# Kernel tuning notes

Hardware: AMD Instinct MI355X
Metric: run time of the kernel (lower is better)

Reference implementation:

```python
import jax, jax.numpy as jnp
import numpy as np

N = 50000          # nodes
E = 1600000        # edges (avg degree 32)
B = 64             # graphs in batch
IN_CH = 128
HEADS = 8
HD = 8             # head_dim = ceil(64/8)
GH = HEADS * HD    # 64 = gat_hidden_dim
HIDDEN = 64
NC = 10
NEG_SLOPE = 0.2
BN_EPS = 1e-5
SIGMA = 0.5


def setup_inputs() -> dict:
    key = jax.random.key(0)
    ks = jax.random.split(key, 24)
    s = 0.1
    inp = {
        "x": jax.random.normal(ks[0], (N, IN_CH), jnp.float32),
        "raw_x": jax.random.uniform(ks[1], (N, 3), jnp.float32),
        "edge_index": jax.random.randint(ks[2], (2, E), 0, N, jnp.int32),
        "batch": jnp.sort(jax.random.randint(ks[3], (N,), 0, B, jnp.int32)),
        # conv1 (heads=8, out=8, edge_dim=1)
        "W1": jax.random.normal(ks[4], (IN_CH, GH), jnp.float32) * s,
        "att_src1": jax.random.normal(ks[5], (HEADS, HD), jnp.float32) * s,
        "att_dst1": jax.random.normal(ks[6], (HEADS, HD), jnp.float32) * s,
        "We1": jax.random.normal(ks[7], (1, GH), jnp.float32) * s,
        "att_e1": jax.random.normal(ks[8], (HEADS, HD), jnp.float32) * s,
        "b1": jax.random.normal(ks[9], (GH,), jnp.float32) * s,
        "gamma1": jnp.ones((GH,), jnp.float32),
        "beta1": jnp.zeros((GH,), jnp.float32),
        "rm1": jax.random.normal(ks[10], (GH,), jnp.float32) * s,
        "rv1": jax.random.uniform(ks[11], (GH,), jnp.float32) + 0.5,
        # conv2 (heads=1, out=64, edge_dim=1)
        "W2": jax.random.normal(ks[12], (GH, HIDDEN), jnp.float32) * s,
        "att_src2": jax.random.normal(ks[13], (1, HIDDEN), jnp.float32) * s,
        "att_dst2": jax.random.normal(ks[14], (1, HIDDEN), jnp.float32) * s,
        "We2": jax.random.normal(ks[15], (1, HIDDEN), jnp.float32) * s,
        "att_e2": jax.random.normal(ks[16], (1, HIDDEN), jnp.float32) * s,
        "b2": jax.random.normal(ks[17], (HIDDEN,), jnp.float32) * s,
        "gamma2": jnp.ones((HIDDEN,), jnp.float32),
        "beta2": jnp.zeros((HIDDEN,), jnp.float32),
        "rm2": jax.random.normal(ks[18], (HIDDEN,), jnp.float32) * s,
        "rv2": jax.random.uniform(ks[19], (HIDDEN,), jnp.float32) + 0.5,
        # classifier
        "Wc": jax.random.normal(ks[20], (HIDDEN, NC), jnp.float32) * s,
        "bc": jax.random.normal(ks[21], (NC,), jnp.float32) * s,
    }
    return inp


def _gat_conv(x, src, dst, edge_attr, W, a_src, a_dst, W_e, a_e, bias, heads, out_ch, n):
    """PyG GATConv (concat=True, add_self_loops=True, fill_value='mean', eval mode)."""
    e0 = edge_attr.shape[0]
    # self-loop edge_attr = mean of incoming edge_attr per node (0 if isolated)
    cnt = jax.ops.segment_sum(jnp.ones((e0,), x.dtype), dst, num_segments=n)
    loop_attr = jax.ops.segment_sum(edge_attr, dst, num_segments=n) / jnp.maximum(cnt, 1.0)[:, None]
    loops = jnp.arange(n, dtype=src.dtype)
    src2 = jnp.concatenate([src, loops])
    dst2 = jnp.concatenate([dst, loops])
    ea = jnp.concatenate([edge_attr, loop_attr], axis=0)          # [E2, 1]
    h = (x @ W).reshape(n, heads, out_ch)                          # [N, H, D]
    al_s = (h * a_src).sum(-1)                                     # [N, H]
    al_d = (h * a_dst).sum(-1)                                     # [N, H]
    al_e = ((ea @ W_e).reshape(-1, heads, out_ch) * a_e).sum(-1)   # [E2, H]
    logits = al_s[src2] + al_d[dst2] + al_e                        # [E2, H]
    logits = jnp.where(logits >= 0, logits, NEG_SLOPE * logits)    # leaky_relu
    # segment softmax over destination nodes (every node has a self loop)
    m = jax.ops.segment_max(logits, dst2, num_segments=n)
    ex = jnp.exp(logits - m[dst2])
    alpha = ex / jax.ops.segment_sum(ex, dst2, num_segments=n)[dst2]
    out = jax.ops.segment_sum(h[src2] * alpha[:, :, None], dst2, num_segments=n)
    return out.reshape(n, heads * out_ch) + bias


def _bn_eval(x, gamma, beta, rm, rv):
    return (x - rm) * (gamma / jnp.sqrt(rv + BN_EPS)) + beta


def reference(x, raw_x, edge_index, batch,
              W1, att_src1, att_dst1, We1, att_e1, b1, gamma1, beta1, rm1, rv1,
              W2, att_src2, att_dst2, We2, att_e2, b2, gamma2, beta2, rm2, rv2,
              Wc, bc):
    src, dst = edge_index[0], edge_index[1]
    # gaussian edge weights from raw features
    diff = raw_x[src] - raw_x[dst]
    dist2 = (diff * diff).sum(axis=1)
    edge_w = jnp.exp(-dist2 / (2.0 * SIGMA * SIGMA))[:, None]      # [E, 1]
    # eval mode: dropout is identity
    h = _gat_conv(x, src, dst, edge_w, W1, att_src1, att_dst1, We1, att_e1, b1, HEADS, HD, N)
    h = jax.nn.elu(_bn_eval(h, gamma1, beta1, rm1, rv1))
    h = _gat_conv(h, src, dst, edge_w, W2, att_src2, att_dst2, We2, att_e2, b2, 1, HIDDEN, N)
    h = jax.nn.elu(_bn_eval(h, gamma2, beta2, rm2, rv2))
    # global mean pool over graphs
    cnt = jax.ops.segment_sum(jnp.ones((N,), h.dtype), batch, num_segments=B)
    g = jax.ops.segment_sum(h, batch, num_segments=B) / jnp.maximum(cnt, 1.0)[:, None]
    return g @ Wc + bc
```

## Files before the change

kernel.cpp:

```cpp
#include <hip/hip_runtime.h>
#include <math.h>

#define N_NODES 50000
#define N_EDGES 1600000
#define NBATCH  64
#define INCH    128
#define HEADS   8
#define HD      8
#define GH      64
#define HIDDEN  64
#define NC      10
#define NEG_SLOPE 0.2f
#define BN_EPS  1e-5f

#define SCAN_TPB 1024
#define NTILES   ((N_NODES + SCAN_TPB - 1) / SCAN_TPB)

typedef unsigned short ushort_t;
typedef unsigned int uint_t;

__device__ __forceinline__ ushort_t f2bf(float f) {
  uint_t u = __float_as_uint(f);
  uint_t r = (u + 0x7fffu + ((u >> 16) & 1u)) >> 16;
  return (ushort_t)r;
}
__device__ __forceinline__ float2 upk(uint_t u) {
  return make_float2(__uint_as_float(u << 16), __uint_as_float(u & 0xffff0000u));
}

__global__ __launch_bounds__(256) void edge_kernel(
    const int* __restrict__ ei, const float* __restrict__ raw,
    float* __restrict__ ea, float* __restrict__ easum, int* __restrict__ cnt) {
  int e = blockIdx.x * blockDim.x + threadIdx.x;
  if (e >= N_EDGES) return;
  int s = ei[e], d = ei[N_EDGES + e];
  float dx = raw[s*3+0] - raw[d*3+0];
  float dy = raw[s*3+1] - raw[d*3+1];
  float dz = raw[s*3+2] - raw[d*3+2];
  float w = __expf(-2.0f * (dx*dx + dy*dy + dz*dz));
  ea[e] = w;
  atomicAdd(&easum[d], w);
  atomicAdd(&cnt[d], 1);
}

__global__ __launch_bounds__(SCAN_TPB) void scan_part(
    const int* __restrict__ cnt, const float* __restrict__ easum,
    int* __restrict__ rowptr, float* __restrict__ loopat, int* __restrict__ bsum) {
  __shared__ int s[SCAN_TPB];
  int t = threadIdx.x;
  int i = blockIdx.x * SCAN_TPB + t;
  int v = (i < N_NODES) ? cnt[i] : 0;
  s[t] = v; __syncthreads();
  for (int off = 1; off < SCAN_TPB; off <<= 1) {
    int u = (t >= off) ? s[t - off] : 0;
    __syncthreads();
    s[t] += u;
    __syncthreads();
  }
  if (i < N_NODES) {
    rowptr[i] = s[t] - v;
    loopat[i] = easum[i] / fmaxf((float)v, 1.0f);
  }
  if (t == SCAN_TPB - 1) bsum[blockIdx.x] = s[t];
}

__global__ __launch_bounds__(64) void scan_top(int* __restrict__ bsum, int* __restrict__ rowptr) {
  int t = threadIdx.x;
  int v = (t < NTILES) ? bsum[t] : 0;
  int orig = v;
  for (int off = 1; off < 64; off <<= 1) {
    int u = __shfl_up(v, off);
    if (t >= off) v += u;
  }
  if (t < NTILES) bsum[t] = v - orig;
  if (t == 0) rowptr[N_NODES] = N_EDGES;
}

__global__ __launch_bounds__(SCAN_TPB) void scan_add(int* __restrict__ rowptr, const int* __restrict__ bsum) {
  int i = blockIdx.x * SCAN_TPB + threadIdx.x;
  if (i < N_NODES) rowptr[i] += bsum[blockIdx.x];
}

__global__ __launch_bounds__(256) void scatter_kernel(
    const int* __restrict__ ei, const float* __restrict__ ea,
    const int* __restrict__ rowptr, int* __restrict__ cnt2,
    int* __restrict__ csr_src, float* __restrict__ csr_ea) {
  int e = blockIdx.x * blockDim.x + threadIdx.x;
  if (e >= N_EDGES) return;
  int s = ei[e], d = ei[N_EDGES + e];
  int pos = rowptr[d] + atomicAdd(&cnt2[d], 1);
  csr_src[pos] = s;
  csr_ea[pos] = ea[e];
}

__global__ __launch_bounds__(256) void gemm1_kernel(
    const float* __restrict__ x, const float* __restrict__ W1,
    const float* __restrict__ asrc, const float* __restrict__ adst,
    ushort_t* __restrict__ h1b, float* __restrict__ als, float* __restrict__ ald) {
  __shared__ float w[INCH * GH];
  for (int i = threadIdx.x; i < INCH * GH / 4; i += blockDim.x)
    ((float4*)w)[i] = ((const float4*)W1)[i];
  __syncthreads();
  int lane = threadIdx.x & 63;
  int waveG = __builtin_amdgcn_readfirstlane((blockIdx.x * blockDim.x + threadIdx.x) >> 6);
  int nWaves = (gridDim.x * blockDim.x) >> 6;
  float a_s = asrc[lane];
  float a_d = adst[lane];
  for (int base = waveG * 4; base < N_NODES; base += nWaves * 4) {
    float acc[4] = {0.f, 0.f, 0.f, 0.f};
    #pragma unroll 8
    for (int k = 0; k < INCH; ++k) {
      float wv = w[k * GH + lane];
      #pragma unroll
      for (int j = 0; j < 4; ++j)
        acc[j] = fmaf(x[(size_t)(base + j) * INCH + k], wv, acc[j]);
    }
    #pragma unroll
    for (int j = 0; j < 4; ++j) {
      int n = base + j;
      float hv = acc[j];
      h1b[(size_t)n * GH + lane] = f2bf(hv);
      float ps = hv * a_s, pd = hv * a_d;
      ps += __shfl_xor(ps, 1); ps += __shfl_xor(ps, 2); ps += __shfl_xor(ps, 4);
      pd += __shfl_xor(pd, 1); pd += __shfl_xor(pd, 2); pd += __shfl_xor(pd, 4);
      if ((lane & 7) == 0) {
        als[n * HEADS + (lane >> 3)] = ps;
        ald[n * HEADS + (lane >> 3)] = pd;
      }
    }
  }
}

__global__ __launch_bounds__(256) void conv1_kernel(
    const ushort_t* __restrict__ h1b, const float* __restrict__ als,
    const float* __restrict__ ald,
    const float* __restrict__ We, const float* __restrict__ ae,
    const int* __restrict__ rowptr,
    const int* __restrict__ csr_src, const float* __restrict__ csr_ea,
    const float* __restrict__ loopat, const float* __restrict__ bias,
    const float* __restrict__ gamma, const float* __restrict__ beta,
    const float* __restrict__ rm, const float* __restrict__ rv,
    float* __restrict__ h2) {
  __shared__ int   src_lds[4][64];
  __shared__ float ea_lds[4][64];
  int l = threadIdx.x & 63;
  int w = threadIdx.x >> 6;
  int n = blockIdx.x * 4 + w;
  if (n >= N_NODES) return;
  int i = l & 15;
  int q = l >> 4;
  int head = i >> 1;
  float4 we4 = ((const float4*)We)[i];
  float4 ae4 = ((const float4*)ae)[i];
  float ce = we4.x*ae4.x + we4.y*ae4.y + we4.z*ae4.z + we4.w*ae4.w;
  ce += __shfl_xor(ce, 1);
  float aldn = ald[(size_t)n * HEADS + head];
  float als_self = als[(size_t)n * HEADS + head];
  const uint2* tab = (const uint2*)h1b;
  uint2 uself = tab[(size_t)n * 16 + i];
  float2 s01 = upk(uself.x), s23 = upk(uself.y);
  int jb = rowptr[n], je = rowptr[n + 1];
  float ssum = 0.f;
  float a0 = 0.f, a1 = 0.f, a2 = 0.f, a3 = 0.f;

#define C1_LOADS(J, R, A, E)                                           \
  {                                                                    \
    int jj = (J);                                                      \
    bool vv = jj < cnt;                                                \
    int ss = vv ? src_lds[w][jj] : 0;                                  \
    R = tab[(size_t)ss * 16 + i];                                      \
    A = vv ? als[(size_t)ss * HEADS + head] : -1e30f;                  \
    E = vv ? ea_lds[w][jj] : 0.f;                                      \
  }
#define C1_LOADG(GI, R0,R1,R2,R3, A0,A1,A2,A3, E0,E1,E2,E3)            \
  {                                                                    \
    int jbase = (GI) * 16 + q;                                         \
    C1_LOADS(jbase,      R0, A0, E0)                                   \
    C1_LOADS(jbase + 4,  R1, A1, E1)                                   \
    C1_LOADS(jbase + 8,  R2, A2, E2)                                   \
    C1_LOADS(jbase + 12, R3, A3, E3)                                   \
  }
#define C1_PROC(R, A, E)                                               \
  {                                                                    \
    float2 t01 = upk(R.x), t23 = upk(R.y);                             \
    float lg = A + aldn + E * ce;                                      \
    lg = (lg >= 0.f) ? lg : NEG_SLOPE * lg;                            \
    float p = __expf(fminf(lg, 60.f));                                 \
    ssum += p;                                                         \
    a0 = fmaf(p, t01.x, a0); a1 = fmaf(p, t01.y, a1);                  \
    a2 = fmaf(p, t23.x, a2); a3 = fmaf(p, t23.y, a3);                  \
  }

  for (int cb = jb; cb < je; cb += 64) {
    int cnt = je - cb; if (cnt > 64) cnt = 64;
    src_lds[w][l] = (l < cnt) ? csr_src[cb + l] : 0;
    ea_lds[w][l]  = (l < cnt) ? csr_ea[cb + l] : 0.f;
    int ng = (cnt + 15) >> 4;
    uint2 rA0, rA1, rA2, rA3, rB0, rB1, rB2, rB3;
    float aA0, aA1, aA2, aA3, aB0, aB1, aB2, aB3;
    float eA0, eA1, eA2, eA3, eB0, eB1, eB2, eB3;
    C1_LOADG(0, rA0,rA1,rA2,rA3, aA0,aA1,aA2,aA3, eA0,eA1,eA2,eA3)
    for (int gi = 0; gi < ng; gi += 2) {
      bool hasB = (gi + 1) < ng;
      if (hasB) C1_LOADG(gi + 1, rB0,rB1,rB2,rB3, aB0,aB1,aB2,aB3, eB0,eB1,eB2,eB3)
      C1_PROC(rA0, aA0, eA0) C1_PROC(rA1, aA1, eA1)
      C1_PROC(rA2, aA2, eA2) C1_PROC(rA3, aA3, eA3)
      if (hasB) {
        if (gi + 2 < ng) C1_LOADG(gi + 2, rA0,rA1,rA2,rA3, aA0,aA1,aA2,aA3, eA0,eA1,eA2,eA3)
        C1_PROC(rB0, aB0, eB0) C1_PROC(rB1, aB1, eB1)
        C1_PROC(rB2, aB2, eB2) C1_PROC(rB3, aB3, eB3)
      }
    }
  }
#undef C1_LOADS
#undef C1_LOADG
#undef C1_PROC

  ssum += __shfl_xor(ssum, 16); ssum += __shfl_xor(ssum, 32);
  a0 += __shfl_xor(a0, 16); a0 += __shfl_xor(a0, 32);
  a1 += __shfl_xor(a1, 16); a1 += __shfl_xor(a1, 32);
  a2 += __shfl_xor(a2, 16); a2 += __shfl_xor(a2, 32);
  a3 += __shfl_xor(a3, 16); a3 += __shfl_xor(a3, 32);
  {
    float lg = als_self + aldn + loopat[n] * ce;
    lg = (lg >= 0.f) ? lg : NEG_SLOPE * lg;
    float p = __expf(fminf(lg, 60.f));
    ssum += p;
    a0 = fmaf(p, s01.x, a0); a1 = fmaf(p, s01.y, a1);
    a2 = fmaf(p, s23.x, a2); a3 = fmaf(p, s23.y, a3);
  }
  if (q == 0) {
    float inv = 1.0f / ssum;
    float4 b4 = ((const float4*)bias)[i];
    float4 g4 = ((const float4*)gamma)[i];
    float4 be4 = ((const float4*)beta)[i];
    float4 rm4 = ((const float4*)rm)[i];
    float4 rv4 = ((const float4*)rv)[i];
    float o0 = a0 * inv + b4.x, o1 = a1 * inv + b4.y;
    float o2 = a2 * inv + b4.z, o3 = a3 * inv + b4.w;
    o0 = (o0 - rm4.x) * (g4.x * rsqrtf(rv4.x + BN_EPS)) + be4.x;
    o1 = (o1 - rm4.y) * (g4.y * rsqrtf(rv4.y + BN_EPS)) + be4.y;
    o2 = (o2 - rm4.z) * (g4.z * rsqrtf(rv4.z + BN_EPS)) + be4.z;
    o3 = (o3 - rm4.w) * (g4.w * rsqrtf(rv4.w + BN_EPS)) + be4.w;
    o0 = (o0 > 0.f) ? o0 : expm1f(o0);
    o1 = (o1 > 0.f) ? o1 : expm1f(o1);
    o2 = (o2 > 0.f) ? o2 : expm1f(o2);
    o3 = (o3 > 0.f) ? o3 : expm1f(o3);
    ((float4*)(h2 + (size_t)n * GH))[i] = make_float4(o0, o1, o2, o3);
  }
}

__global__ __launch_bounds__(256) void gemm2_kernel(
    const float* __restrict__ x, const float* __restrict__ W2,
    const float* __restrict__ asrc, const float* __restrict__ adst,
    ushort_t* __restrict__ h2mb, float* __restrict__ als, float* __restrict__ ald) {
  __shared__ float w[HIDDEN * HIDDEN];
  for (int i = threadIdx.x; i < HIDDEN * HIDDEN / 4; i += blockDim.x)
    ((float4*)w)[i] = ((const float4*)W2)[i];
  __syncthreads();
  int lane = threadIdx.x & 63;
  int waveG = __builtin_amdgcn_readfirstlane((blockIdx.x * blockDim.x + threadIdx.x) >> 6);
  int nWaves = (gridDim.x * blockDim.x) >> 6;
  float a_s = asrc[lane];
  float a_d = adst[lane];
  for (int base = waveG * 4; base < N_NODES; base += nWaves * 4) {
    float acc[4] = {0.f, 0.f, 0.f, 0.f};
    #pragma unroll 8
    for (int k = 0; k < HIDDEN; ++k) {
      float wv = w[k * HIDDEN + lane];
      #pragma unroll
      for (int j = 0; j < 4; ++j)
        acc[j] = fmaf(x[(size_t)(base + j) * HIDDEN + k], wv, acc[j]);
    }
    #pragma unroll
    for (int j = 0; j < 4; ++j) {
      int n = base + j;
      float hv = acc[j];
      h2mb[(size_t)n * HIDDEN + lane] = f2bf(hv);
      float ps = hv * a_s, pd = hv * a_d;
      #pragma unroll
      for (int off = 1; off < 64; off <<= 1) {
        ps += __shfl_xor(ps, off);
        pd += __shfl_xor(pd, off);
      }
      if (lane == 0) { als[n] = ps; ald[n] = pd; }
    }
  }
}

__global__ __launch_bounds__(256) void conv2_kernel(
    const ushort_t* __restrict__ h2mb, const float* __restrict__ als,
    const float* __restrict__ ald,
    const float* __restrict__ We, const float* __restrict__ ae,
    const int* __restrict__ rowptr,
    const int* __restrict__ csr_src, const float* __restrict__ csr_ea,
    const float* __restrict__ loopat, const float* __restrict__ bias,
    const float* __restrict__ gamma, const float* __restrict__ beta,
    const float* __restrict__ rm, const float* __restrict__ rv,
    const int* __restrict__ batch,
    float* __restrict__ pool, int* __restrict__ cntg) {
  __shared__ int   src_lds[4][64];
  __shared__ float ea_lds[4][64];
  int l = threadIdx.x & 63;
  int w = threadIdx.x >> 6;
  int n = blockIdx.x * 4 + w;
  if (n >= N_NODES) return;
  int i = l & 15;
  int q = l >> 4;
  float4 we4 = ((const float4*)We)[i];
  float4 ae4 = ((const float4*)ae)[i];
  float ce = we4.x*ae4.x + we4.y*ae4.y + we4.z*ae4.z + we4.w*ae4.w;
  ce += __shfl_xor(ce, 1); ce += __shfl_xor(ce, 2);
  ce += __shfl_xor(ce, 4); ce += __shfl_xor(ce, 8);
  float aldn = ald[n];
  float als_self = als[n];
  const uint2* tab = (const uint2*)h2mb;
  uint2 uself = tab[(size_t)n * 16 + i];
  float2 s01 = upk(uself.x), s23 = upk(uself.y);
  int jb = rowptr[n], je = rowptr[n + 1];
  float ssum = 0.f;
  float a0 = 0.f, a1 = 0.f, a2 = 0.f, a3 = 0.f;

#define C2_LOADS(J, R, A, E)                                           \
  {                                                                    \
    int jj = (J);                                                      \
    bool vv = jj < cnt;                                                \
    int ss = vv ? src_lds[w][jj] : 0;                                  \
    R = tab[(size_t)ss * 16 + i];                                      \
    A = vv ? als[ss] : -1e30f;                                         \
    E = vv ? ea_lds[w][jj] : 0.f;                                      \
  }
#define C2_LOADG(GI, R0,R1,R2,R3, A0,A1,A2,A3, E0,E1,E2,E3)            \
  {                                                                    \
    int jbase = (GI) * 16 + q;                                         \
    C2_LOADS(jbase,      R0, A0, E0)                                   \
    C2_LOADS(jbase + 4,  R1, A1, E1)                                   \
    C2_LOADS(jbase + 8,  R2, A2, E2)                                   \
    C2_LOADS(jbase + 12, R3, A3, E3)                                   \
  }
#define C2_PROC(R, A, E)                                               \
  {                                                                    \
    float2 t01 = upk(R.x), t23 = upk(R.y);                             \
    float lg = A + aldn + E * ce;                                      \
    lg = (lg >= 0.f) ? lg : NEG_SLOPE * lg;                            \
    float p = __expf(fminf(lg, 60.f));                                 \
    ssum += p;                                                         \
    a0 = fmaf(p, t01.x, a0); a1 = fmaf(p, t01.y, a1);                  \
    a2 = fmaf(p, t23.x, a2); a3 = fmaf(p, t23.y, a3);                  \
  }

  for (int cb = jb; cb < je; cb += 64) {
    int cnt = je - cb; if (cnt > 64) cnt = 64;
    src_lds[w][l] = (l < cnt) ? csr_src[cb + l] : 0;
    ea_lds[w][l]  = (l < cnt) ? csr_ea[cb + l] : 0.f;
    int ng = (cnt + 15) >> 4;
    uint2 rA0, rA1, rA2, rA3, rB0, rB1, rB2, rB3;
    float aA0, aA1, aA2, aA3, aB0, aB1, aB2, aB3;
    float eA0, eA1, eA2, eA3, eB0, eB1, eB2, eB3;
    C2_LOADG(0, rA0,rA1,rA2,rA3, aA0,aA1,aA2,aA3, eA0,eA1,eA2,eA3)
    for (int gi = 0; gi < ng; gi += 2) {
      bool hasB = (gi + 1) < ng;
      if (hasB) C2_LOADG(gi + 1, rB0,rB1,rB2,rB3, aB0,aB1,aB2,aB3, eB0,eB1,eB2,eB3)
      C2_PROC(rA0, aA0, eA0) C2_PROC(rA1, aA1, eA1)
      C2_PROC(rA2, aA2, eA2) C2_PROC(rA3, aA3, eA3)
      if (hasB) {
        if (gi + 2 < ng) C2_LOADG(gi + 2, rA0,rA1,rA2,rA3, aA0,aA1,aA2,aA3, eA0,eA1,eA2,eA3)
        C2_PROC(rB0, aB0, eB0) C2_PROC(rB1, aB1, eB1)
        C2_PROC(rB2, aB2, eB2) C2_PROC(rB3, aB3, eB3)
      }
    }
  }
#undef C2_LOADS
#undef C2_LOADG
#undef C2_PROC

  ssum += __shfl_xor(ssum, 16); ssum += __shfl_xor(ssum, 32);
  a0 += __shfl_xor(a0, 16); a0 += __shfl_xor(a0, 32);
  a1 += __shfl_xor(a1, 16); a1 += __shfl_xor(a1, 32);
  a2 += __shfl_xor(a2, 16); a2 += __shfl_xor(a2, 32);
  a3 += __shfl_xor(a3, 16); a3 += __shfl_xor(a3, 32);
  {
    float lg = als_self + aldn + loopat[n] * ce;
    lg = (lg >= 0.f) ? lg : NEG_SLOPE * lg;
    float p = __expf(fminf(lg, 60.f));
    ssum += p;
    a0 = fmaf(p, s01.x, a0); a1 = fmaf(p, s01.y, a1);
    a2 = fmaf(p, s23.x, a2); a3 = fmaf(p, s23.y, a3);
  }
  if (q == 0) {
    float inv = 1.0f / ssum;
    float4 b4 = ((const float4*)bias)[i];
    float4 g4 = ((const float4*)gamma)[i];
    float4 be4 = ((const float4*)beta)[i];
    float4 rm4 = ((const float4*)rm)[i];
    float4 rv4 = ((const float4*)rv)[i];
    float o0 = a0 * inv + b4.x, o1 = a1 * inv + b4.y;
    float o2 = a2 * inv + b4.z, o3 = a3 * inv + b4.w;
    o0 = (o0 - rm4.x) * (g4.x * rsqrtf(rv4.x + BN_EPS)) + be4.x;
    o1 = (o1 - rm4.y) * (g4.y * rsqrtf(rv4.y + BN_EPS)) + be4.y;
    o2 = (o2 - rm4.z) * (g4.z * rsqrtf(rv4.z + BN_EPS)) + be4.z;
    o3 = (o3 - rm4.w) * (g4.w * rsqrtf(rv4.w + BN_EPS)) + be4.w;
    o0 = (o0 > 0.f) ? o0 : expm1f(o0);
    o1 = (o1 > 0.f) ? o1 : expm1f(o1);
    o2 = (o2 > 0.f) ? o2 : expm1f(o2);
    o3 = (o3 > 0.f) ? o3 : expm1f(o3);
    int b = batch[n];
    float* pp = pool + (size_t)b * HIDDEN + 4 * i;
    atomicAdd(pp + 0, o0);
    atomicAdd(pp + 1, o1);
    atomicAdd(pp + 2, o2);
    atomicAdd(pp + 3, o3);
    if (l == 0) atomicAdd(&cntg[b], 1);
  }
}

__global__ __launch_bounds__(640) void final_kernel(
    const float* __restrict__ pool, const int* __restrict__ cntg,
    const float* __restrict__ Wc, const float* __restrict__ bc,
    float* __restrict__ out) {
  int t = threadIdx.x;
  if (t >= NBATCH * NC) return;
  int b = t / NC, c = t - b * NC;
  float inv = 1.0f / fmaxf((float)cntg[b], 1.0f);
  float s = bc[c];
  #pragma unroll
  for (int d = 0; d < HIDDEN; ++d)
    s = fmaf(pool[b * HIDDEN + d] * inv, Wc[d * NC + c], s);
  out[t] = s;
}

extern "C" void kernel_launch(void* const* d_in, const int* in_sizes, int n_in,
                              void* d_out, int out_size, void* d_ws, size_t ws_size,
                              hipStream_t stream) {
  const float* x     = (const float*)d_in[0];
  const float* raw   = (const float*)d_in[1];
  const int*   ei    = (const int*)  d_in[2];
  const int*   batch = (const int*)  d_in[3];
  const float* W1    = (const float*)d_in[4];
  const float* asrc1 = (const float*)d_in[5];
  const float* adst1 = (const float*)d_in[6];
  const float* We1   = (const float*)d_in[7];
  const float* ae1   = (const float*)d_in[8];
  const float* b1    = (const float*)d_in[9];
  const float* g1    = (const float*)d_in[10];
  const float* be1   = (const float*)d_in[11];
  const float* rm1   = (const float*)d_in[12];
  const float* rv1   = (const float*)d_in[13];
  const float* W2    = (const float*)d_in[14];
  const float* asrc2 = (const float*)d_in[15];
  const float* adst2 = (const float*)d_in[16];
  const float* We2   = (const float*)d_in[17];
  const float* ae2   = (const float*)d_in[18];
  const float* b2    = (const float*)d_in[19];
  const float* g2    = (const float*)d_in[20];
  const float* be2   = (const float*)d_in[21];
  const float* rm2   = (const float*)d_in[22];
  const float* rv2   = (const float*)d_in[23];
  const float* Wc    = (const float*)d_in[24];
  const float* bc    = (const float*)d_in[25];
  float* out = (float*)d_out;

  char* ws = (char*)d_ws;
  size_t off = 0;
  auto alloc = [&](size_t bytes) -> void* {
    void* p = ws + off;
    off += bytes;
    off = (off + 255) & ~(size_t)255;
    return p;
  };
  float*    ea      = (float*)   alloc((size_t)N_EDGES * 4);
  float*    csr_ea  = (float*)   alloc((size_t)N_EDGES * 4);
  int*      csr_src = (int*)     alloc((size_t)N_EDGES * 4);
  float*    easum   = (float*)   alloc((size_t)N_NODES * 4);
  int*      cnt     = (int*)     alloc((size_t)N_NODES * 4);
  int*      cnt2    = (int*)     alloc((size_t)N_NODES * 4);
  int*      rowptr  = (int*)     alloc((size_t)(N_NODES + 1) * 4);
  float*    loopat  = (float*)   alloc((size_t)N_NODES * 4);
  ushort_t* h1b     = (ushort_t*)alloc((size_t)N_NODES * GH * 2);
  float*    als1    = (float*)   alloc((size_t)N_NODES * HEADS * 4);
  float*    ald1    = (float*)   alloc((size_t)N_NODES * HEADS * 4);
  float*    h2      = (float*)   alloc((size_t)N_NODES * GH * 4);
  ushort_t* h2mb    = (ushort_t*)alloc((size_t)N_NODES * HIDDEN * 2);
  float*    als2    = (float*)   alloc((size_t)N_NODES * 4);
  float*    ald2    = (float*)   alloc((size_t)N_NODES * 4);
  int*      bsum    = (int*)     alloc(64 * 4);
  float*    pool    = (float*)   alloc((size_t)NBATCH * HIDDEN * 4);
  int*      cntg    = (int*)     alloc((size_t)NBATCH * 4);

  hipMemsetAsync(easum, 0, (size_t)N_NODES * 4, stream);
  hipMemsetAsync(cnt,   0, (size_t)N_NODES * 4, stream);
  hipMemsetAsync(cnt2,  0, (size_t)N_NODES * 4, stream);
  hipMemsetAsync(pool,  0, (size_t)NBATCH * HIDDEN * 4, stream);
  hipMemsetAsync(cntg,  0, (size_t)NBATCH * 4, stream);

  int egrid = (N_EDGES + 255) / 256;
  edge_kernel<<<egrid, 256, 0, stream>>>(ei, raw, ea, easum, cnt);
  scan_part<<<NTILES, SCAN_TPB, 0, stream>>>(cnt, easum, rowptr, loopat, bsum);
  scan_top<<<1, 64, 0, stream>>>(bsum, rowptr);
  scan_add<<<NTILES, SCAN_TPB, 0, stream>>>(rowptr, bsum);
  scatter_kernel<<<egrid, 256, 0, stream>>>(ei, ea, rowptr, cnt2, csr_src, csr_ea);

  gemm1_kernel<<<1024, 256, 0, stream>>>(x, W1, asrc1, adst1, h1b, als1, ald1);
  conv1_kernel<<<(N_NODES + 3) / 4, 256, 0, stream>>>(h1b, als1, ald1, We1, ae1,
      rowptr, csr_src, csr_ea, loopat, b1, g1, be1, rm1, rv1, h2);
  gemm2_kernel<<<1024, 256, 0, stream>>>(h2, W2, asrc2, adst2, h2mb, als2, ald2);
  conv2_kernel<<<(N_NODES + 3) / 4, 256, 0, stream>>>(h2mb, als2, ald2, We2, ae2,
      rowptr, csr_src, csr_ea, loopat, b2, g2, be2, rm2, rv2, batch, pool, cntg);
  final_kernel<<<1, 640, 0, stream>>>(pool, cntg, Wc, bc, out);
}
```

Measured before the change: 1.005 ms.

## Split feature gather tables into halves and run conv passes per half

The bf16 node feature tables are split into two 32-column halves, and each GAT aggregation kernel runs twice, once per half. The aim is to shrink the randomly gathered table from 6.4MB to 3.2MB per pass so it fits better in the L2/LLC, cutting miss traffic on neighbor gathers. In exchange, the CSR indices, edge attributes and attention logits are read twice, and each pass recomputes the softmax denominator.

```diff
diff --git a/kernel.cpp b/kernel.cpp
--- a/kernel.cpp
+++ b/kernel.cpp
@@ -96,7 +96,8 @@
 __global__ __launch_bounds__(256) void gemm1_kernel(
     const float* __restrict__ x, const float* __restrict__ W1,
     const float* __restrict__ asrc, const float* __restrict__ adst,
-    ushort_t* __restrict__ h1b, float* __restrict__ als, float* __restrict__ ald) {
+    ushort_t* __restrict__ tabLo, ushort_t* __restrict__ tabHi,
+    float* __restrict__ als, float* __restrict__ ald) {
   __shared__ float w[INCH * GH];
   for (int i = threadIdx.x; i < INCH * GH / 4; i += blockDim.x)
     ((float4*)w)[i] = ((const float4*)W1)[i];
@@ -119,7 +120,9 @@
     for (int j = 0; j < 4; ++j) {
       int n = base + j;
       float hv = acc[j];
-      h1b[(size_t)n * GH + lane] = f2bf(hv);
+      ushort_t hb = f2bf(hv);
+      if (lane < 32) tabLo[(size_t)n * 32 + lane] = hb;
+      else           tabHi[(size_t)n * 32 + (lane - 32)] = hb;
       float ps = hv * a_s, pd = hv * a_d;
       ps += __shfl_xor(ps, 1); ps += __shfl_xor(ps, 2); ps += __shfl_xor(ps, 4);
       pd += __shfl_xor(pd, 1); pd += __shfl_xor(pd, 2); pd += __shfl_xor(pd, 4);
@@ -131,8 +134,8 @@
   }
 }
 
-__global__ __launch_bounds__(256) void conv1_kernel(
-    const ushort_t* __restrict__ h1b, const float* __restrict__ als,
+__global__ __launch_bounds__(256) void conv1_half_kernel(
+    const ushort_t* __restrict__ tab, const float* __restrict__ als,
     const float* __restrict__ ald,
     const float* __restrict__ We, const float* __restrict__ ae,
     const int* __restrict__ rowptr,
@@ -140,47 +143,40 @@
     const float* __restrict__ loopat, const float* __restrict__ bias,
     const float* __restrict__ gamma, const float* __restrict__ beta,
     const float* __restrict__ rm, const float* __restrict__ rv,
-    float* __restrict__ h2) {
+    float* __restrict__ h2, int H) {
   __shared__ int   src_lds[4][64];
   __shared__ float ea_lds[4][64];
   int l = threadIdx.x & 63;
   int w = threadIdx.x >> 6;
   int n = blockIdx.x * 4 + w;
   if (n >= N_NODES) return;
-  int i = l & 15;
-  int q = l >> 4;
-  int head = i >> 1;
-  float4 we4 = ((const float4*)We)[i];
-  float4 ae4 = ((const float4*)ae)[i];
+  int i8 = l & 7;
+  int oct = l >> 3;
+  int fidx = H * 8 + i8;
+  int head = H * 4 + (i8 >> 1);
+  float4 we4 = ((const float4*)We)[fidx];
+  float4 ae4 = ((const float4*)ae)[fidx];
   float ce = we4.x*ae4.x + we4.y*ae4.y + we4.z*ae4.z + we4.w*ae4.w;
   ce += __shfl_xor(ce, 1);
-  float aldn = ald[(size_t)n * HEADS + head];
+  float aldn     = ald[(size_t)n * HEADS + head];
   float als_self = als[(size_t)n * HEADS + head];
-  const uint2* tab = (const uint2*)h1b;
-  uint2 uself = tab[(size_t)n * 16 + i];
+  const uint2* tb = (const uint2*)tab;
+  uint2 uself = tb[(size_t)n * 8 + i8];
   float2 s01 = upk(uself.x), s23 = upk(uself.y);
   int jb = rowptr[n], je = rowptr[n + 1];
   float ssum = 0.f;
   float a0 = 0.f, a1 = 0.f, a2 = 0.f, a3 = 0.f;
 
-#define C1_LOADS(J, R, A, E)                                           \
+#define CH1_LOADG(G, R, A, E)                                          \
   {                                                                    \
-    int jj = (J);                                                      \
+    int jj = (G) * 8 + oct;                                            \
     bool vv = jj < cnt;                                                \
     int ss = vv ? src_lds[w][jj] : 0;                                  \
-    R = tab[(size_t)ss * 16 + i];                                      \
+    R = tb[(size_t)ss * 8 + i8];                                       \
     A = vv ? als[(size_t)ss * HEADS + head] : -1e30f;                  \
     E = vv ? ea_lds[w][jj] : 0.f;                                      \
   }
-#define C1_LOADG(GI, R0,R1,R2,R3, A0,A1,A2,A3, E0,E1,E2,E3)            \
-  {                                                                    \
-    int jbase = (GI) * 16 + q;                                         \
-    C1_LOADS(jbase,      R0, A0, E0)                                   \
-    C1_LOADS(jbase + 4,  R1, A1, E1)                                   \
-    C1_LOADS(jbase + 8,  R2, A2, E2)                                   \
-    C1_LOADS(jbase + 12, R3, A3, E3)                                   \
-  }
-#define C1_PROC(R, A, E)                                               \
+#define CH1_PROC(R, A, E)                                              \
   {                                                                    \
     float2 t01 = upk(R.x), t23 = upk(R.y);                             \
     float lg = A + aldn + E * ce;                                      \
@@ -195,32 +191,27 @@
     int cnt = je - cb; if (cnt > 64) cnt = 64;
     src_lds[w][l] = (l < cnt) ? csr_src[cb + l] : 0;
     ea_lds[w][l]  = (l < cnt) ? csr_ea[cb + l] : 0.f;
-    int ng = (cnt + 15) >> 4;
-    uint2 rA0, rA1, rA2, rA3, rB0, rB1, rB2, rB3;
-    float aA0, aA1, aA2, aA3, aB0, aB1, aB2, aB3;
-    float eA0, eA1, eA2, eA3, eB0, eB1, eB2, eB3;
-    C1_LOADG(0, rA0,rA1,rA2,rA3, aA0,aA1,aA2,aA3, eA0,eA1,eA2,eA3)
-    for (int gi = 0; gi < ng; gi += 2) {
-      bool hasB = (gi + 1) < ng;
-      if (hasB) C1_LOADG(gi + 1, rB0,rB1,rB2,rB3, aB0,aB1,aB2,aB3, eB0,eB1,eB2,eB3)
-      C1_PROC(rA0, aA0, eA0) C1_PROC(rA1, aA1, eA1)
-      C1_PROC(rA2, aA2, eA2) C1_PROC(rA3, aA3, eA3)
+    int ng = (cnt + 7) >> 3;
+    uint2 rA, rB; float aA, aB, eA, eB;
+    CH1_LOADG(0, rA, aA, eA)
+    for (int g = 0; g < ng; g += 2) {
+      bool hasB = (g + 1) < ng;
+      if (hasB) CH1_LOADG(g + 1, rB, aB, eB)
+      CH1_PROC(rA, aA, eA)
       if (hasB) {
-        if (gi + 2 < ng) C1_LOADG(gi + 2, rA0,rA1,rA2,rA3, aA0,aA1,aA2,aA3, eA0,eA1,eA2,eA3)
-        C1_PROC(rB0, aB0, eB0) C1_PROC(rB1, aB1, eB1)
-        C1_PROC(rB2, aB2, eB2) C1_PROC(rB3, aB3, eB3)
+        if (g + 2 < ng) CH1_LOADG(g + 2, rA, aA, eA)
+        CH1_PROC(rB, aB, eB)
       }
     }
   }
-#undef C1_LOADS
-#undef C1_LOADG
-#undef C1_PROC
-
-  ssum += __shfl_xor(ssum, 16); ssum += __shfl_xor(ssum, 32);
-  a0 += __shfl_xor(a0, 16); a0 += __shfl_xor(a0, 32);
-  a1 += __shfl_xor(a1, 16); a1 += __shfl_xor(a1, 32);
-  a2 += __shfl_xor(a2, 16); a2 += __shfl_xor(a2, 32);
-  a3 += __shfl_xor(a3, 16); a3 += __shfl_xor(a3, 32);
+#undef CH1_LOADG
+#undef CH1_PROC
+
+  ssum += __shfl_xor(ssum, 8); ssum += __shfl_xor(ssum, 16); ssum += __shfl_xor(ssum, 32);
+  a0 += __shfl_xor(a0, 8); a0 += __shfl_xor(a0, 16); a0 += __shfl_xor(a0, 32);
+  a1 += __shfl_xor(a1, 8); a1 += __shfl_xor(a1, 16); a1 += __shfl_xor(a1, 32);
+  a2 += __shfl_xor(a2, 8); a2 += __shfl_xor(a2, 16); a2 += __shfl_xor(a2, 32);
+  a3 += __shfl_xor(a3, 8); a3 += __shfl_xor(a3, 16); a3 += __shfl_xor(a3, 32);
   {
     float lg = als_self + aldn + loopat[n] * ce;
     lg = (lg >= 0.f) ? lg : NEG_SLOPE * lg;
@@ -229,13 +220,13 @@
     a0 = fmaf(p, s01.x, a0); a1 = fmaf(p, s01.y, a1);
     a2 = fmaf(p, s23.x, a2); a3 = fmaf(p, s23.y, a3);
   }
-  if (q == 0) {
+  if (oct == 0) {
     float inv = 1.0f / ssum;
-    float4 b4 = ((const float4*)bias)[i];
-    float4 g4 = ((const float4*)gamma)[i];
-    float4 be4 = ((const float4*)beta)[i];
-    float4 rm4 = ((const float4*)rm)[i];
-    float4 rv4 = ((const float4*)rv)[i];
+    float4 b4 = ((const float4*)bias)[fidx];
+    float4 g4 = ((const float4*)gamma)[fidx];
+    float4 be4 = ((const float4*)beta)[fidx];
+    float4 rm4 = ((const float4*)rm)[fidx];
+    float4 rv4 = ((const float4*)rv)[fidx];
     float o0 = a0 * inv + b4.x, o1 = a1 * inv + b4.y;
     float o2 = a2 * inv + b4.z, o3 = a3 * inv + b4.w;
     o0 = (o0 - rm4.x) * (g4.x * rsqrtf(rv4.x + BN_EPS)) + be4.x;
@@ -246,14 +237,15 @@
     o1 = (o1 > 0.f) ? o1 : expm1f(o1);
     o2 = (o2 > 0.f) ? o2 : expm1f(o2);
     o3 = (o3 > 0.f) ? o3 : expm1f(o3);
-    ((float4*)(h2 + (size_t)n * GH))[i] = make_float4(o0, o1, o2, o3);
+    ((float4*)(h2 + (size_t)n * GH))[fidx] = make_float4(o0, o1, o2, o3);
   }
 }
 
 __global__ __launch_bounds__(256) void gemm2_kernel(
     const float* __restrict__ x, const float* __restrict__ W2,
     const float* __restrict__ asrc, const float* __restrict__ adst,
-    ushort_t* __restrict__ h2mb, float* __restrict__ als, float* __restrict__ ald) {
+    ushort_t* __restrict__ tabLo, ushort_t* __restrict__ tabHi,
+    float* __restrict__ als, float* __restrict__ ald) {
   __shared__ float w[HIDDEN * HIDDEN];
   for (int i = threadIdx.x; i < HIDDEN * HIDDEN / 4; i += blockDim.x)
     ((float4*)w)[i] = ((const float4*)W2)[i];
@@ -276,7 +268,9 @@
     for (int j = 0; j < 4; ++j) {
       int n = base + j;
       float hv = acc[j];
-      h2mb[(size_t)n * HIDDEN + lane] = f2bf(hv);
+      ushort_t hb = f2bf(hv);
+      if (lane < 32) tabLo[(size_t)n * 32 + lane] = hb;
+      else           tabHi[(size_t)n * 32 + (lane - 32)] = hb;
       float ps = hv * a_s, pd = hv * a_d;
       #pragma unroll
       for (int off = 1; off < 64; off <<= 1) {
@@ -288,8 +282,8 @@
   }
 }
 
-__global__ __launch_bounds__(256) void conv2_kernel(
-    const ushort_t* __restrict__ h2mb, const float* __restrict__ als,
+__global__ __launch_bounds__(256) void conv2_half_kernel(
+    const ushort_t* __restrict__ tab, const float* __restrict__ als,
     const float* __restrict__ ald,
     const float* __restrict__ We, const float* __restrict__ ae,
     const int* __restrict__ rowptr,
@@ -298,47 +292,42 @@
     const float* __restrict__ gamma, const float* __restrict__ beta,
     const float* __restrict__ rm, const float* __restrict__ rv,
     const int* __restrict__ batch,
-    float* __restrict__ pool, int* __restrict__ cntg) {
+    float* __restrict__ pool, int* __restrict__ cntg, int H) {
   __shared__ int   src_lds[4][64];
   __shared__ float ea_lds[4][64];
   int l = threadIdx.x & 63;
   int w = threadIdx.x >> 6;
   int n = blockIdx.x * 4 + w;
   if (n >= N_NODES) return;
-  int i = l & 15;
-  int q = l >> 4;
-  float4 we4 = ((const float4*)We)[i];
-  float4 ae4 = ((const float4*)ae)[i];
-  float ce = we4.x*ae4.x + we4.y*ae4.y + we4.z*ae4.z + we4.w*ae4.w;
-  ce += __shfl_xor(ce, 1); ce += __shfl_xor(ce, 2);
-  ce += __shfl_xor(ce, 4); ce += __shfl_xor(ce, 8);
-  float aldn = ald[n];
+  int i8 = l & 7;
+  int oct = l >> 3;
+  int fidx = H * 8 + i8;
+  float4 wa = ((const float4*)We)[i8];
+  float4 aa = ((const float4*)ae)[i8];
+  float4 wb = ((const float4*)We)[i8 + 8];
+  float4 ab = ((const float4*)ae)[i8 + 8];
+  float ce = wa.x*aa.x + wa.y*aa.y + wa.z*aa.z + wa.w*aa.w
+           + wb.x*ab.x + wb.y*ab.y + wb.z*ab.z + wb.w*ab.w;
+  ce += __shfl_xor(ce, 1); ce += __shfl_xor(ce, 2); ce += __shfl_xor(ce, 4);
+  float aldn     = ald[n];
   float als_self = als[n];
-  const uint2* tab = (const uint2*)h2mb;
-  uint2 uself = tab[(size_t)n * 16 + i];
+  const uint2* tb = (const uint2*)tab;
+  uint2 uself = tb[(size_t)n * 8 + i8];
   float2 s01 = upk(uself.x), s23 = upk(uself.y);
   int jb = rowptr[n], je = rowptr[n + 1];
   float ssum = 0.f;
   float a0 = 0.f, a1 = 0.f, a2 = 0.f, a3 = 0.f;
 
-#define C2_LOADS(J, R, A, E)                                           \
+#define CH2_LOADG(G, R, A, E)                                          \
   {                                                                    \
-    int jj = (J);                                                      \
+    int jj = (G) * 8 + oct;                                            \
     bool vv = jj < cnt;                                                \
     int ss = vv ? src_lds[w][jj] : 0;                                  \
-    R = tab[(size_t)ss * 16 + i];                                      \
+    R = tb[(size_t)ss * 8 + i8];                                       \
     A = vv ? als[ss] : -1e30f;                                         \
     E = vv ? ea_lds[w][jj] : 0.f;                                      \
   }
-#define C2_LOADG(GI, R0,R1,R2,R3, A0,A1,A2,A3, E0,E1,E2,E3)            \
-  {                                                                    \
-    int jbase = (GI) * 16 + q;                                         \
-    C2_LOADS(jbase,      R0, A0, E0)                                   \
-    C2_LOADS(jbase + 4,  R1, A1, E1)                                   \
-    C2_LOADS(jbase + 8,  R2, A2, E2)                                   \
-    C2_LOADS(jbase + 12, R3, A3, E3)                                   \
-  }
-#define C2_PROC(R, A, E)                                               \
+#define CH2_PROC(R, A, E)                                              \
   {                                                                    \
     float2 t01 = upk(R.x), t23 = upk(R.y);                             \
     float lg = A + aldn + E * ce;                                      \
@@ -353,32 +342,27 @@
     int cnt = je - cb; if (cnt > 64) cnt = 64;
     src_lds[w][l] = (l < cnt) ? csr_src[cb + l] : 0;
     ea_lds[w][l]  = (l < cnt) ? csr_ea[cb + l] : 0.f;
-    int ng = (cnt + 15) >> 4;
-    uint2 rA0, rA1, rA2, rA3, rB0, rB1, rB2, rB3;
-    float aA0, aA1, aA2, aA3, aB0, aB1, aB2, aB3;
-    float eA0, eA1, eA2, eA3, eB0, eB1, eB2, eB3;
-    C2_LOADG(0, rA0,rA1,rA2,rA3, aA0,aA1,aA2,aA3, eA0,eA1,eA2,eA3)
-    for (int gi = 0; gi < ng; gi += 2) {
-      bool hasB = (gi + 1) < ng;
-      if (hasB) C2_LOADG(gi + 1, rB0,rB1,rB2,rB3, aB0,aB1,aB2,aB3, eB0,eB1,eB2,eB3)
-      C2_PROC(rA0, aA0, eA0) C2_PROC(rA1, aA1, eA1)
-      C2_PROC(rA2, aA2, eA2) C2_PROC(rA3, aA3, eA3)
+    int ng = (cnt + 7) >> 3;
+    uint2 rA, rB; float aA, aB, eA, eB;
+    CH2_LOADG(0, rA, aA, eA)
+    for (int g = 0; g < ng; g += 2) {
+      bool hasB = (g + 1) < ng;
+      if (hasB) CH2_LOADG(g + 1, rB, aB, eB)
+      CH2_PROC(rA, aA, eA)
       if (hasB) {
-        if (gi + 2 < ng) C2_LOADG(gi + 2, rA0,rA1,rA2,rA3, aA0,aA1,aA2,aA3, eA0,eA1,eA2,eA3)
-        C2_PROC(rB0, aB0, eB0) C2_PROC(rB1, aB1, eB1)
-        C2_PROC(rB2, aB2, eB2) C2_PROC(rB3, aB3, eB3)
+        if (g + 2 < ng) CH2_LOADG(g + 2, rA, aA, eA)
+        CH2_PROC(rB, aB, eB)
       }
     }
   }
-#undef C2_LOADS
-#undef C2_LOADG
-#undef C2_PROC
-
-  ssum += __shfl_xor(ssum, 16); ssum += __shfl_xor(ssum, 32);
-  a0 += __shfl_xor(a0, 16); a0 += __shfl_xor(a0, 32);
-  a1 += __shfl_xor(a1, 16); a1 += __shfl_xor(a1, 32);
-  a2 += __shfl_xor(a2, 16); a2 += __shfl_xor(a2, 32);
-  a3 += __shfl_xor(a3, 16); a3 += __shfl_xor(a3, 32);
+#undef CH2_LOADG
+#undef CH2_PROC
+
+  ssum += __shfl_xor(ssum, 8); ssum += __shfl_xor(ssum, 16); ssum += __shfl_xor(ssum, 32);
+  a0 += __shfl_xor(a0, 8); a0 += __shfl_xor(a0, 16); a0 += __shfl_xor(a0, 32);
+  a1 += __shfl_xor(a1, 8); a1 += __shfl_xor(a1, 16); a1 += __shfl_xor(a1, 32);
+  a2 += __shfl_xor(a2, 8); a2 += __shfl_xor(a2, 16); a2 += __shfl_xor(a2, 32);
+  a3 += __shfl_xor(a3, 8); a3 += __shfl_xor(a3, 16); a3 += __shfl_xor(a3, 32);
   {
     float lg = als_self + aldn + loopat[n] * ce;
     lg = (lg >= 0.f) ? lg : NEG_SLOPE * lg;
@@ -387,13 +371,13 @@
     a0 = fmaf(p, s01.x, a0); a1 = fmaf(p, s01.y, a1);
     a2 = fmaf(p, s23.x, a2); a3 = fmaf(p, s23.y, a3);
   }
-  if (q == 0) {
+  if (oct == 0) {
     float inv = 1.0f / ssum;
-    float4 b4 = ((const float4*)bias)[i];
-    float4 g4 = ((const float4*)gamma)[i];
-    float4 be4 = ((const float4*)beta)[i];
-    float4 rm4 = ((const float4*)rm)[i];
-    float4 rv4 = ((const float4*)rv)[i];
+    float4 b4 = ((const float4*)bias)[fidx];
+    float4 g4 = ((const float4*)gamma)[fidx];
+    float4 be4 = ((const float4*)beta)[fidx];
+    float4 rm4 = ((const float4*)rm)[fidx];
+    float4 rv4 = ((const float4*)rv)[fidx];
     float o0 = a0 * inv + b4.x, o1 = a1 * inv + b4.y;
     float o2 = a2 * inv + b4.z, o3 = a3 * inv + b4.w;
     o0 = (o0 - rm4.x) * (g4.x * rsqrtf(rv4.x + BN_EPS)) + be4.x;
@@ -405,12 +389,12 @@
     o2 = (o2 > 0.f) ? o2 : expm1f(o2);
     o3 = (o3 > 0.f) ? o3 : expm1f(o3);
     int b = batch[n];
-    float* pp = pool + (size_t)b * HIDDEN + 4 * i;
+    float* pp = pool + (size_t)b * HIDDEN + H * 32 + 4 * i8;
     atomicAdd(pp + 0, o0);
     atomicAdd(pp + 1, o1);
     atomicAdd(pp + 2, o2);
     atomicAdd(pp + 3, o3);
-    if (l == 0) atomicAdd(&cntg[b], 1);
+    if (H == 0 && l == 0) atomicAdd(&cntg[b], 1);
   }
 }
 
@@ -476,11 +460,13 @@
   int*      cnt2    = (int*)     alloc((size_t)N_NODES * 4);
   int*      rowptr  = (int*)     alloc((size_t)(N_NODES + 1) * 4);
   float*    loopat  = (float*)   alloc((size_t)N_NODES * 4);
-  ushort_t* h1b     = (ushort_t*)alloc((size_t)N_NODES * GH * 2);
+  ushort_t* tabLo1  = (ushort_t*)alloc((size_t)N_NODES * 32 * 2);
+  ushort_t* tabHi1  = (ushort_t*)alloc((size_t)N_NODES * 32 * 2);
   float*    als1    = (float*)   alloc((size_t)N_NODES * HEADS * 4);
   float*    ald1    = (float*)   alloc((size_t)N_NODES * HEADS * 4);
   float*    h2      = (float*)   alloc((size_t)N_NODES * GH * 4);
-  ushort_t* h2mb    = (ushort_t*)alloc((size_t)N_NODES * HIDDEN * 2);
+  ushort_t* tabLo2  = (ushort_t*)alloc((size_t)N_NODES * 32 * 2);
+  ushort_t* tabHi2  = (ushort_t*)alloc((size_t)N_NODES * 32 * 2);
   float*    als2    = (float*)   alloc((size_t)N_NODES * 4);
   float*    ald2    = (float*)   alloc((size_t)N_NODES * 4);
   int*      bsum    = (int*)     alloc(64 * 4);
@@ -500,11 +486,16 @@
   scan_add<<<NTILES, SCAN_TPB, 0, stream>>>(rowptr, bsum);
   scatter_kernel<<<egrid, 256, 0, stream>>>(ei, ea, rowptr, cnt2, csr_src, csr_ea);
 
-  gemm1_kernel<<<1024, 256, 0, stream>>>(x, W1, asrc1, adst1, h1b, als1, ald1);
-  conv1_kernel<<<(N_NODES + 3) / 4, 256, 0, stream>>>(h1b, als1, ald1, We1, ae1,
-      rowptr, csr_src, csr_ea, loopat, b1, g1, be1, rm1, rv1, h2);
-  gemm2_kernel<<<1024, 256, 0, stream>>>(h2, W2, asrc2, adst2, h2mb, als2, ald2);
-  conv2_kernel<<<(N_NODES + 3) / 4, 256, 0, stream>>>(h2mb, als2, ald2, We2, ae2,
-      rowptr, csr_src, csr_ea, loopat, b2, g2, be2, rm2, rv2, batch, pool, cntg);
+  int cgrid = (N_NODES + 3) / 4;
+  gemm1_kernel<<<1024, 256, 0, stream>>>(x, W1, asrc1, adst1, tabLo1, tabHi1, als1, ald1);
+  conv1_half_kernel<<<cgrid, 256, 0, stream>>>(tabLo1, als1, ald1, We1, ae1,
+      rowptr, csr_src, csr_ea, loopat, b1, g1, be1, rm1, rv1, h2, 0);
+  conv1_half_kernel<<<cgrid, 256, 0, stream>>>(tabHi1, als1, ald1, We1, ae1,
+      rowptr, csr_src, csr_ea, loopat, b1, g1, be1, rm1, rv1, h2, 1);
+  gemm2_kernel<<<1024, 256, 0, stream>>>(h2, W2, asrc2, adst2, tabLo2, tabHi2, als2, ald2);
+  conv2_half_kernel<<<cgrid, 256, 0, stream>>>(tabLo2, als2, ald2, We2, ae2,
+      rowptr, csr_src, csr_ea, loopat, b2, g2, be2, rm2, rv2, batch, pool, cntg, 0);
+  conv2_half_kernel<<<cgrid, 256, 0, stream>>>(tabHi2, als2, ald2, We2, ae2,
+      rowptr, csr_src, csr_ea, loopat, b2, g2, be2, rm2, rv2, batch, pool, cntg, 1);
   final_kernel<<<1, 640, 0, stream>>>(pool, cntg, Wc, bc, out);
 }
```

Result: slower. 1.104 ms (+9.8%).
